# Kernel tuning notes

Measured on AMD Instinct MI355X. Metric: run time of the kernel, lower is better.

## Reference

```python
import jax, jax.numpy as jnp
import numpy as np

B, S, D, H = 64, 65536, 512, 256
H2 = H // 2
CAP_LIMIT = 0.85
ACT_THR = 0.5


def _normalize(x):
    return x / jnp.maximum(jnp.linalg.norm(x, axis=-1, keepdims=True), 1e-12)


def _layernorm(x, g, b):
    m = x.mean(-1, keepdims=True)
    v = ((x - m) ** 2).mean(-1, keepdims=True)
    return (x - m) / jnp.sqrt(v + 1e-5) * g + b


def setup_inputs() -> dict:
    key = jax.random.key(0)
    ks = jax.random.split(key, 20)

    def lin(k, i, o):
        s = 1.0 / np.sqrt(i)
        kw, kb = jax.random.split(k)
        return (jax.random.uniform(kw, (i, o), minval=-s, maxval=s),
                jax.random.uniform(kb, (o,), minval=-s, maxval=s))

    inp = {}
    inp["new_content"] = jax.random.normal(ks[0], (B, D), dtype=jnp.float32)
    inp["query"] = jax.random.normal(ks[1], (B, D), dtype=jnp.float32)
    inp["memory_bank"] = jax.random.normal(ks[2], (S, D), dtype=jnp.float32)
    inp["access_times"] = jax.random.uniform(ks[3], (S,), minval=0.0, maxval=900.0)
    inp["current_step"] = 1000
    inp["sr_w1"], inp["sr_b1"] = lin(ks[4], 2 * D, H)
    inp["sr_g"] = jnp.ones((H,), jnp.float32)
    inp["sr_beta"] = jnp.zeros((H,), jnp.float32)
    inp["sr_w2"], inp["sr_b2"] = lin(ks[5], H, H2)
    inp["sn_w"], inp["sn_b"] = lin(ks[6], D, H2)
    inp["sg_w"], inp["sg_b"] = lin(ks[7], H2, 1)
    inp["el_w"], inp["el_b"] = lin(ks[8], 1, 32)
    inp["ec_w"], inp["ec_b"] = lin(ks[9], D, 32)
    inp["eg_w"], inp["eg_b"] = lin(ks[10], 64, 1)
    inp["dd_w1"], inp["dd_b1"] = lin(ks[11], 2 * D, H)
    inp["dd_w2"], inp["dd_b2"] = lin(ks[12], H, 1)
    inp["ds_w1"], inp["ds_b1"] = lin(ks[13], 2 * D, H)
    inp["ds_w2"], inp["ds_b2"] = lin(ks[14], H, 1)
    return inp


def _forward(new_content, query, memory_bank, access_times,
             sr_w1, sr_b1, sr_g, sr_beta, sr_w2, sr_b2,
             sn_w, sn_b, sg_w, sg_b,
             el_w, el_b, ec_w, ec_b, eg_w, eg_b,
             dd_w1, dd_b1, dd_w2, dd_b2,
             ds_w1, ds_b1, ds_w2, ds_b2,
             step):
    mem = memory_bank
    at = access_times
    norms = jnp.linalg.norm(mem, axis=-1)               # [S]
    capacity = jnp.mean((norms > ACT_THR).astype(jnp.float32))
    dyn_thr = jnp.clip(
        jnp.where(capacity < 0.3, 0.08,
                  jnp.where(capacity < 0.6, 0.08 + (capacity - 0.3) * 0.733,
                            0.3 + (capacity - 0.6))), 0.0, 0.7)
    topk_thr = jnp.where(capacity < 0.3, 0.1, jnp.where(capacity < 0.6, 0.2, 0.4))
    raw_thr = jnp.where(capacity < 0.3, 0.3, 0.5)

    # store relevance / novelty / gate
    combined = jnp.concatenate([new_content, query], -1)          # [B,2D]
    h = _layernorm(combined @ sr_w1 + sr_b1, sr_g, sr_beta)
    rel = jax.nn.relu(jax.nn.relu(h) @ sr_w2 + sr_b2)             # [B,H2]
    nn_ = _normalize(new_content)
    sims = nn_ @ _normalize(mem).T                                # [B,S]
    max_sim = sims.max(-1, keepdims=True)
    novelty = (1.0 - max_sim) / 2.0                               # [B,1]
    nf = jax.nn.sigmoid(new_content @ sn_w + sn_b)
    store_score = jax.nn.sigmoid((rel + nf) @ sg_w + sg_b)        # [B,1]

    # novelty percentile over active slots (no boolean-shape gather)
    active = norms > ACT_THR
    n_active = active.sum()
    nov_mean = novelty.mean()
    cond = (nov_mean > (1.0 - sims)) & active[None, :]
    denom = (new_content.shape[0] * jnp.maximum(n_active, 1)).astype(jnp.float32)
    perc = jnp.where(n_active > 0, cond.sum().astype(jnp.float32) / denom, 1.0)

    base_store = store_score.mean() > raw_thr
    novelty_ok = nov_mean > dyn_thr
    topk_ok = perc > topk_thr
    should_store = base_store & novelty_ok & topk_ok

    # emergency erase (capacity over limit)
    do_erase = capacity > CAP_LIMIT
    age = jnp.maximum(step - at, 0.0)
    es_em = age / (age.max() + 1e-6) + (1.0 - jax.nn.sigmoid(norms))
    victim = jnp.argmax(es_em)
    mem = jnp.where(do_erase, mem.at[victim].set(0.0), mem)
    at = jnp.where(do_erase, at.at[victim].set(-99999.0), at)
    should_store = should_store & jnp.logical_not(do_erase & jnp.logical_not(novelty_ok))

    # per-slot erase scores
    lru = jax.nn.relu(((step - at) / 1000.0)[:, None] @ el_w + el_b)   # [S,32]
    conf = jax.nn.sigmoid(mem @ ec_w + ec_b)                            # [S,32]
    erase_scores = jax.nn.sigmoid(jnp.concatenate([lru, conf], -1) @ eg_w + eg_b)[:, 0]

    # conflict detection: top-3 similar slots, gather-MLP-scatter drift
    sims2 = _normalize(new_content) @ _normalize(mem).T                # [B,S]
    tv, ti = jax.lax.top_k(sims2, 3)                                   # [B,3]
    cmask = (tv > 0.7) & (tv < 0.99)
    gathered = mem[ti]                                                 # [B,3,D]
    pair = jnp.concatenate([jnp.broadcast_to(new_content[:, None, :], gathered.shape), gathered], -1)
    prob = jax.nn.sigmoid(jax.nn.relu(pair @ dd_w1 + dd_b1) @ dd_w2 + dd_b2)[..., 0]
    strength = jax.nn.sigmoid(jax.nn.relu(pair @ ds_w1 + ds_b1) @ ds_w2 + ds_b2)[..., 0]
    apply_m = cmask & (prob > 0.5)                                     # [B,3]
    avg = (new_content[:, None, :] + gathered) / 2.0
    s = strength[..., None]
    dn_cand = (1.0 - s) * new_content[:, None, :] + s * avg
    do_cand = (1.0 - s) * gathered + s * avg
    drifted_new = new_content
    for k in range(3):  # fixed k=3, later k overwrites (matches torch inner loop)
        drifted_new = jnp.where(apply_m[:, k:k + 1], dn_cand[:, k], drifted_new)
    for k in range(3):
        idx = ti[:, k]
        cur = mem[idx]
        mem = mem.at[idx].set(jnp.where(apply_m[:, k, None], do_cand[:, k], cur))

    # conditional write
    slot_age = step - at
    recent = (at >= 0.0) & (slot_age < 3.0)
    masked = erase_scores * (~recent).astype(erase_scores.dtype)
    masked = jnp.where(masked.max() <= 0.0, slot_age, masked)
    write_idx = jnp.where(do_erase, victim, jnp.argmax(masked))
    erase_out = jnp.where(should_store & jnp.logical_not(do_erase), masked, erase_scores)
    mem = jnp.where(should_store, mem.at[write_idx].set(drifted_new[0]), mem)
    at = jnp.where(should_store, at.at[write_idx].set(step), at)

    recent_changes = jnp.abs(mem - memory_bank).mean()
    return (mem, at, erase_out, store_score[:, 0], novelty[:, 0], recent_changes)


def reference(new_content, query, memory_bank, access_times,
              sr_w1, sr_b1, sr_g, sr_beta, sr_w2, sr_b2,
              sn_w, sn_b, sg_w, sg_b,
              el_w, el_b, ec_w, ec_b, eg_w, eg_b,
              dd_w1, dd_b1, dd_w2, dd_b2,
              ds_w1, ds_b1, ds_w2, ds_b2,
              current_step):
    step = jnp.float32(current_step)
    return _forward(new_content, query, memory_bank, access_times,
                    sr_w1, sr_b1, sr_g, sr_beta, sr_w2, sr_b2,
                    sn_w, sn_b, sg_w, sg_b,
                    el_w, el_b, ec_w, ec_b, eg_w, eg_b,
                    dd_w1, dd_b1, dd_w2, dd_b2,
                    ds_w1, ds_b1, ds_w2, ds_b2, step)
```

## Files before the change

### kernel.cpp

```cpp
#include <hip/hip_runtime.h>
#include <math.h>
#include <limits.h>

#define S_N 65536
#define D_N 512
#define B_N 64

typedef __attribute__((ext_vector_type(8))) short short8;
typedef __attribute__((ext_vector_type(4))) float f32x4;

#define SIMS_F      (B_N*S_N/2)
#define OFF_SIMS    0
#define OFF_AEXT    (OFF_SIMS + SIMS_F)
#define AEXT_F      (96*512/2)
#define OFF_NORMS   (OFF_AEXT + AEXT_F)
#define OFF_CONF    (OFF_NORMS + S_N)
#define OFF_FLAGS   (OFF_CONF + S_N)
#define OFF_LIST    (OFF_FLAGS + S_N)
#define OFF_MASKED  (OFF_LIST + 256)
#define OFF_ERSC    (OFF_MASKED + S_N)
#define OFF_SLOTAGE (OFF_ERSC + S_N)
#define OFF_STORES  (OFF_SLOTAGE + S_N)
#define OFF_MAXSIM  (OFF_STORES + 64)
#define OFF_TI      (OFF_MAXSIM + 64)
// ... 55 lines not shown
__device__ __forceinline__ void touch_row(int row, float* ws){
  int* flags = (int*)(ws + OFF_FLAGS);
  if (atomicExch(&flags[row], 1) == 0){
    Scal* sc = (Scal*)(ws + OFF_SCAL);
    int i = atomicAdd(&sc->list_cnt, 1);
    ((int*)(ws + OFF_LIST))[i] = row;
  }
}

__device__ __forceinline__ void gld16(const float* g, void* l){
  __builtin_amdgcn_global_load_lds((const __attribute__((address_space(1))) void*)g,
                                   (__attribute__((address_space(3))) void*)l, 16, 0, 0);
}
#define WAITV(N) asm volatile("s_waitcnt vmcnt(" #N ")" ::: "memory")

__global__ __launch_bounds__(256) void k_init(const float* __restrict__ nc,
                                              const float* __restrict__ at_in,
                                              const float* __restrict__ ec_w,
                                              const int* __restrict__ step_p,
                                              float* __restrict__ ws, float* __restrict__ out){
  int blk = blockIdx.x, t = threadIdx.x;
  Scal* sc = (Scal*)(ws + OFF_SCAL);
  unsigned short* aB = (unsigned short*)(ws + OFF_AEXT);
  if (blk == 0){
    if (t == 0){
      sc->victim_pack = 0ULL; sc->masked_pack = 0ULL; sc->slotage_pack = 0ULL;
      sc->cnt_active = 0; sc->cond_cnt = 0; sc->age_max_t = 0u;
      sc->nov_mean = 0.0f; sc->changed_sum = 0.0f;
      sc->do_erase = 0; sc->should_store = 0; sc->write_idx = 0; sc->victim_idx = 0;
      sc->list_cnt = 0;
    }
    if (t < 64) ((unsigned*)(ws + OFF_MAXSIM))[t] = 0u;
  } else if (blk <= 64){
    int b = blk - 1;
    __shared__ float red[256];
    float x0 = nc[b*512 + t], x1 = nc[b*512 + 256 + t];
    red[t] = x0*x0 + x1*x1;
    __syncthreads();
    for (int o=128;o>0;o>>=1){ if (t<o) red[t]+=red[t+o]; __syncthreads(); }
    float inv = 1.0f / fmaxf(sqrtf(red[0]), 1e-12f);
    aB[b*512 + t]       = bf16r(x0*inv);
    aB[b*512 + 256 + t] = bf16r(x1*inv);
  } else if (blk <= 96){
    int j = blk - 65;
    for (int d=t; d<512; d+=256) aB[(64+j)*512 + d] = bf16r(ec_w[d*32 + j]);
  } else if (blk <= 160){
    int part = blk - 97;
    float stepf = (float)step_p[0];
    float lmax = -1e30f;
    for (int s = part*1024 + t; s < (part+1)*1024; s += 256)
      lmax = fmaxf(lmax, fmaxf(stepf - at_in[s], 0.0f));
    __shared__ float red[256];
    red[t]=lmax; __syncthreads();
    for (int o=128;o>0;o>>=1){ if (t<o) red[t]=fmaxf(red[t],red[t+o]); __syncthreads(); }
    if (t==0) atomicMax(&sc->age_max_t, f2mono(red[0]));
  } else if (blk <= 224){
    int part = blk - 161;
    for (int s = part*1024 + t; s < (part+1)*1024; s += 256)
      out[OUT_AT + s] = at_in[s];
  } else {
    int part = blk - 225;
    int* flags = (int*)(ws + OFF_FLAGS);
    for (int s = part*1024 + t; s < (part+1)*1024; s += 256) flags[s] = 0;
  }
}

__global__ __launch_bounds__(256) void k_phase1(const float* __restrict__ mem,
                                                const float* __restrict__ ec_b,
                                                const float* __restrict__ eg_w,
                                                float* __restrict__ ws, float* __restrict__ out){
  __shared__ __align__(16) unsigned short aT[96*520];
  __shared__ __align__(16) char chunks[4*4*2048];
  __shared__ unsigned lmax[64];
  int t = threadIdx.x;
  int s0 = blockIdx.x * 64;
  Scal* sc = (Scal*)(ws + OFF_SCAL);
  int lane = t & 63, wv = t >> 6;
  int quad = lane >> 4, l15 = lane & 15;
  int row = wv*16 + l15;

  {
    const uint4* src = (const uint4*)(ws + OFF_AEXT);
    #pragma unroll
    for (int i=0;i<24;i++){
      int idx = i*256 + t;
      int arow = idx >> 6, c16 = idx & 63;
      uint4 v = src[idx];
      *(uint4*)((char*)aT + arow*1040 + c16*16) = v;
    }
    if (t < 64) lmax[t] = 0u;
  }
  __syncthreads();

  const float* gsrc = mem + ((size_t)(s0 + row))*512 + quad*8;
  float* od = out + OUT_MEM + ((size_t)(s0 + row))*512 + quad*8;
  char* mybuf = chunks + wv*8192;
  #define STAGE(c) do{ \
    gld16(gsrc + (c)*32,     mybuf + ((c)&3)*2048); \
    gld16(gsrc + (c)*32 + 4, mybuf + ((c)&3)*2048 + 1024); \
  }while(0)

  STAGE(0); asm volatile("" ::: "memory");
  STAGE(1); asm volatile("" ::: "memory");
  STAGE(2); asm volatile("" ::: "memory");

  f32x4 acc[6];
  #pragma unroll
  for (int r=0;r<6;r++) acc[r] = (f32x4){0.f,0.f,0.f,0.f};
  float ssq = 0.f;

  #pragma unroll
  for (int c=0;c<16;c++){
    if (c < 13) STAGE(c+3);
    if      (c == 0)  WAITV(6);
    else if (c == 1)  WAITV(8);
    else if (c == 2)  WAITV(10);
    else if (c <= 12) WAITV(12);
    else if (c == 13) WAITV(10);
    else if (c == 14) WAITV(8);
    else              WAITV(6);
    __builtin_amdgcn_sched_barrier(0);
    const char* bp = mybuf + (c&3)*2048;
    float4 v0 = *(const float4*)(bp + lane*16);
    float4 v1 = *(const float4*)(bp + 1024 + lane*16);
    *(float4*)(od + c*32)     = v0;
    *(float4*)(od + c*32 + 4) = v1;
    ssq = fmaf(v0.x,v0.x,ssq); ssq = fmaf(v0.y,v0.y,ssq);
    ssq = fmaf(v0.z,v0.z,ssq); ssq = fmaf(v0.w,v0.w,ssq);
    ssq = fmaf(v1.x,v1.x,ssq); ssq = fmaf(v1.y,v1.y,ssq);
    ssq = fmaf(v1.z,v1.z,ssq); ssq = fmaf(v1.w,v1.w,ssq);
    short8 bfrag;
    bfrag[0]=(short)bf16r(v0.x); bfrag[1]=(short)bf16r(v0.y);
    bfrag[2]=(short)bf16r(v0.z); bfrag[3]=(short)bf16r(v0.w);
    bfrag[4]=(short)bf16r(v1.x); bfrag[5]=(short)bf16r(v1.y);
    bfrag[6]=(short)bf16r(v1.z); bfrag[7]=(short)bf16r(v1.w);
    #pragma unroll
    for (int rt=0;rt<6;rt++){
      short8 afrag = *(const short8*)&aT[(rt*16 + l15)*520 + c*32 + quad*8];
      acc[rt] = __builtin_amdgcn_mfma_f32_16x16x32_bf16(afrag, bfrag, acc[rt], 0,0,0);
    }
  }
  #undef STAGE

  ssq += __shfl_xor(ssq, 16);
  ssq += __shfl_xor(ssq, 32);
  float nrm = sqrtf(ssq);
  float lv = 1.0f / fmaxf(nrm, 1e-12f);
  if (quad == 0) ws[OFF_NORMS + s0 + row] = nrm;
  unsigned long long m = __ballot(quad==0 && nrm > 0.5f);
  if (lane == 0) atomicAdd(&sc->cnt_active, (int)__popcll(m));

  unsigned short* simsb = (unsigned short*)(ws + OFF_SIMS);
  #pragma unroll
  for (int rt=0;rt<4;rt++){
    #pragma unroll
    for (int r=0;r<4;r++){
      int a = rt*16 + quad*4 + r;
      float sim = acc[rt][r] * lv;
      simsb[(size_t)a*S_N + s0 + row] = bf16r(sim);
      atomicMax(&lmax[a], f2mono(sim));
    }
  }
  float cpart = 0.f;
  #pragma unroll
  for (int rt=4;rt<6;rt++){
    #pragma unroll
    for (int r=0;r<4;r++){
      int j = (rt-4)*16 + quad*4 + r;
      cpart += sigmoidf_(acc[rt][r] + ec_b[j]) * eg_w[32+j];
    }
  }
  cpart += __shfl_down(cpart, 32);
  cpart += __shfl_down(cpart, 16);
  if (lane < 16) ws[OFF_CONF + s0 + row] = cpart;
  __syncthreads();
  if (t < 64) atomicMax(((unsigned*)(ws + OFF_MAXSIM)) + t, lmax[t]);
}

__global__ __launch_bounds__(256) void k_mlp1a(const float* __restrict__ nc, const float* __restrict__ qr,
    const float* __restrict__ sr_w1, float* __restrict__ ws){
  int blk = blockIdx.x, t = threadIdx.x;
  int b = blk >> 1, half = blk & 1;
  __shared__ float ch[512];
  const float* src = half ? qr : nc;
  ch[t] = src[b*512 + t]; ch[256+t] = src[b*512 + 256 + t];
  __syncthreads();
  float h = 0.f;
  const float* w = sr_w1 + (half*512)*256 + t;
  for (int i=0;i<512;i++) h = fmaf(ch[i], w[i*256], h);
  ws[OFF_HM + (half*64 + b)*256 + t] = h;
}

__global__ __launch_bounds__(256) void k_mlp1b(const float* __restrict__ nc, const float* __restrict__ qr,
    const float* __restrict__ sr_b1, const float* __restrict__ sr_g, const float* __restrict__ sr_beta,
    const float* __restrict__ sr_w2, const float* __restrict__ sr_b2,
    const float* __restrict__ sn_w,  const float* __restrict__ sn_b,
    const float* __restrict__ sg_w,  const float* __restrict__ sg_b,
    float* __restrict__ ws, float* __restrict__ out){
  int b = blockIdx.x, t = threadIdx.x;
  Scal* sc = (Scal*)(ws + OFF_SCAL);
  __shared__ float red[256];
  if (b == 64){
    const unsigned* gms = (const unsigned*)(ws + OFF_MAXSIM);
    float nv = 0.0f;
    if (t < 64){
      float msim = mono2f(gms[t]);
      nv = (1.0f - msim) * 0.5f;
      out[OUT_NOV + t] = nv;
    }
    red[t] = (t < 64) ? nv : 0.0f;
    __syncthreads();
    for (int o=128;o>0;o>>=1){ if (t<o) red[t]+=red[t+o]; __syncthreads(); }
    if (t == 0) sc->nov_mean = red[0] / 64.0f;
    return;
  }
  __shared__ float comb[1024];
  __shared__ float hbuf[256];
  comb[t]       = nc[b*512 + t];
  comb[256 + t] = nc[b*512 + 256 + t];
  comb[512 + t] = qr[b*512 + t];
  comb[768 + t] = qr[b*512 + 256 + t];
  float h = ws[OFF_HM + b*256 + t] + ws[OFF_HM + (64 + b)*256 + t] + sr_b1[t];
  red[t] = h; __syncthreads();
  for (int o=128;o>0;o>>=1){ if (t<o) red[t]+=red[t+o]; __syncthreads(); }
  float mean = red[0] / 256.0f;
  __syncthreads();
  float dx = h - mean;
  red[t] = dx*dx; __syncthreads();
  for (int o=128;o>0;o>>=1){ if (t<o) red[t]+=red[t+o]; __syncthreads(); }
  float var = red[0] / 256.0f;
  __syncthreads();
  float hn = dx / sqrtf(var + 1e-5f) * sr_g[t] + sr_beta[t];
  hbuf[t] = fmaxf(hn, 0.0f);
  __syncthreads();
  float val = 0.0f;
  if (t < 128){
    float r = sr_b2[t];
    for (int j=0;j<256;j++) r = fmaf(hbuf[j], sr_w2[j*128 + t], r);
    r = fmaxf(r, 0.0f);
    float nf = sn_b[t];
    for (int d=0; d<512; d++) nf = fmaf(comb[d], sn_w[d*128 + t], nf);
    nf = sigmoidf_(nf);
    val = (r + nf) * sg_w[t];
  }
  red[t] = val; __syncthreads();
  for (int o=128;o>0;o>>=1){ if (t<o) red[t]+=red[t+o]; __syncthreads(); }
  if (t == 0){
    float ssc = sigmoidf_(red[0] + sg_b[0]);
    out[OUT_SS + b] = ssc;
    ws[OFF_STORES + b] = ssc;
  }
}

__global__ __launch_bounds__(256) void k_scan(const float* __restrict__ at_in,
                                              const int* __restrict__ step_p,
                                              float* __restrict__ ws){
  int t = threadIdx.x;
  Scal* sc = (Scal*)(ws + OFF_SCAL);
  float thr = 1.0f - sc->nov_mean;
  float stepf = (float)step_p[0];
  float agemax = mono2f(sc->age_max_t);
  const unsigned* simsu = (const unsigned*)(ws + OFF_SIMS);
  const float* norms = ws + OFF_NORMS;
  int gid = blockIdx.x*256 + t;
  int gstride = gridDim.x*256;
  int cnt = 0;
  for (int idx = gid; idx < B_N*S_N/2; idx += gstride){
    unsigned u = simsu[idx];
    int s = (idx*2) & (S_N-1);
    float v0 = __uint_as_float(u<<16);
    float v1 = __uint_as_float(u & 0xffff0000u);
    if (v0 > thr && norms[s]   > 0.5f) cnt++;
    if (v1 > thr && norms[s+1] > 0.5f) cnt++;
  }
  unsigned long long best = 0ULL;
  for (int s = gid; s < S_N; s += gstride){
    float age = fmaxf(stepf - at_in[s], 0.0f);
    float es = age/(agemax + 1e-6f) + (1.0f - sigmoidf_(norms[s]));
    unsigned long long pk = packvi(es, s);
    if (pk > best) best = pk;
  }
  __shared__ int redc[256];
  __shared__ unsigned long long redp[256];
  redc[t] = cnt; redp[t] = best;
  __syncthreads();
  for (int o=128;o>0;o>>=1){
    if (t<o){ redc[t]+=redc[t+o]; if (redp[t+o] > redp[t]) redp[t]=redp[t+o]; }
    __syncthreads();
  }
  if (t == 0){
    atomicAdd(&sc->cond_cnt, redc[0]);
    atomicMax(&sc->victim_pack, redp[0]);
  }
}

__global__ __launch_bounds__(256) void k_victimfix(const float* __restrict__ ec_b,
                                                   const float* __restrict__ eg_w,
                                                   float* __restrict__ ws, float* __restrict__ out){
  int t = threadIdx.x;
  Scal* sc = (Scal*)(ws + OFF_SCAL);
  float capacity = (float)sc->cnt_active / 65536.0f;
  int de = (capacity > 0.85f) ? 1 : 0;
  int victim = (int)(0xFFFFFFFFu - (unsigned)(sc->victim_pack & 0xFFFFFFFFULL));
  if (t == 0){ sc->do_erase = de; sc->victim_idx = victim; }
  if (de){
    for (int d=t; d<512; d+=256) out[OUT_MEM + victim*512 + d] = 0.0f;
    if (t == 0){
      out[OUT_AT + victim] = -99999.0f;
      touch_row(victim, ws);
      float sum = 0.0f;
      for (int j=0;j<32;j++) sum += sigmoidf_(ec_b[j]) * eg_w[32 + j];
      ws[OFF_CONF + victim] = sum;
    }
  }
}

__global__ __launch_bounds__(256) void k_top3(float* __restrict__ ws){
  int b = blockIdx.x, t = threadIdx.x;
  Scal* sc = (Scal*)(ws + OFF_SCAL);
  int de = sc->do_erase;
  int victim = sc->victim_idx;
  const unsigned short* simrow = (const unsigned short*)(ws + OFF_SIMS) + (size_t)b*S_N;
  float v[3] = {-1e30f,-1e30f,-1e30f};
  int ix[3] = {INT_MAX, INT_MAX, INT_MAX};
  for (int s = t; s < S_N; s += 256){
    float val = bf2f(simrow[s]);
    if (de && s == victim) val = 0.0f;
    if (betterVI(val, s, v[2], ix[2])){
      if (betterVI(val, s, v[1], ix[1])){
        if (betterVI(val, s, v[0], ix[0])){
          v[2]=v[1]; ix[2]=ix[1]; v[1]=v[0]; ix[1]=ix[0]; v[0]=val; ix[0]=s;
        } else { v[2]=v[1]; ix[2]=ix[1]; v[1]=val; ix[1]=s; }
      } else { v[2]=val; ix[2]=s; }
    }
  }
  __shared__ float sv[256*3];
  __shared__ int   si[256*3];
  for (int r=0;r<3;r++){ sv[t*3+r]=v[r]; si[t*3+r]=ix[r]; }
  for (int off=128; off>0; off>>=1){
    __syncthreads();
    if (t < off){
      float av[3], bv[3], ov[3]; int ai[3], bi[3], oi[3];
      for (int r=0;r<3;r++){ av[r]=sv[t*3+r]; ai[r]=si[t*3+r]; bv[r]=sv[(t+off)*3+r]; bi[r]=si[(t+off)*3+r]; }
      int ap=0, bp=0;
      for (int r=0;r<3;r++){
        bool takeA = (bp>=3) || (ap<3 && betterVI(av[ap],ai[ap],bv[bp],bi[bp]));
        if (takeA){ ov[r]=av[ap]; oi[r]=ai[ap]; ap++; }
        else      { ov[r]=bv[bp]; oi[r]=bi[bp]; bp++; }
      }
      for (int r=0;r<3;r++){ sv[t*3+r]=ov[r]; si[t*3+r]=oi[r]; }
    }
  }
  __syncthreads();
  if (t == 0){
    for (int k=0;k<3;k++){
      ws[OFF_TV + b*3 + k] = sv[k];
      ((int*)(ws + OFF_TI))[b*3 + k] = si[k];
    }
  }
}

__global__ __launch_bounds__(256) void k_mlp2(const float* __restrict__ nc,
    const float* __restrict__ dd_w1, const float* __restrict__ ds_w1,
    float* __restrict__ ws, float* __restrict__ out){
  int blk = blockIdx.x, t = threadIdx.x;
  int b = blk >> 2, ks = blk & 3;
  __shared__ float ch[3*256];
  if (ks < 2){
    ch[t] = nc[b*512 + ks*256 + t];
    __syncthreads();
    float hd = 0.f, hs = 0.f;
    const float* wd = dd_w1 + (ks*256)*256 + t;
// ... 62 lines not shown
  float tvv = ws[OFF_TV + p];
  int ap = (tvv > 0.7f && tvv < 0.99f && prob > 0.5f) ? 1 : 0;
  if (t == 0){
    ((int*)(ws + OFF_APPLY))[p] = ap;
    touch_row(row, ws);
  }
  for (int d=t; d<512; d+=256){
    float n = nc[b*512 + d];
    float g = out[OUT_MEM + (size_t)row*512 + d];
    float avg = 0.5f*(n + g);
    ws[OFF_DOCAND + p*512 + d] = (1.0f - stren)*g + stren*avg;
    if (b == 0) ws[OFF_DNC0 + k*512 + d] = (1.0f - stren)*n + stren*avg;
  }
}

__global__ __launch_bounds__(64) void k_scatter(float* __restrict__ ws, float* __restrict__ out){
  int d = blockIdx.x*64 + threadIdx.x;
  const int* tip = (const int*)(ws + OFF_TI);
  const int* ap  = (const int*)(ws + OFF_APPLY);
  for (int k=0;k<3;k++){
    float cur[64];
    #pragma unroll
    for (int b=0;b<64;b++) cur[b] = out[OUT_MEM + (size_t)tip[b*3 + k]*512 + d];
    #pragma unroll
    for (int b=0;b<64;b++){
      int p = b*3 + k;
      float v = ap[p] ? ws[OFF_DOCAND + p*512 + d] : cur[b];
      out[OUT_MEM + (size_t)tip[p]*512 + d] = v;
    }
  }
}

__global__ __launch_bounds__(256) void k_erase(const int* __restrict__ step_p,
    const float* __restrict__ el_w, const float* __restrict__ el_b,
    const float* __restrict__ eg_w, const float* __restrict__ eg_b,
    float* __restrict__ ws, float* __restrict__ out){
  int t = threadIdx.x;
  Scal* sc = (Scal*)(ws + OFF_SCAL);
  float stepf = (float)step_p[0];
  float egb = eg_b[0];
  int gid = blockIdx.x*256 + t;
  int gstride = gridDim.x*256;
  unsigned long long bm = 0ULL, bs = 0ULL;
  for (int s = gid; s < S_N; s += gstride){
    float a = out[OUT_AT + s];
    float x = (stepf - a) / 1000.0f;
    float lp = 0.0f;
    #pragma unroll
    for (int j=0;j<32;j++) lp += fmaxf(x*el_w[j] + el_b[j], 0.0f) * eg_w[j];
    float er = sigmoidf_(lp + ws[OFF_CONF + s] + egb);
    float sa = stepf - a;
    bool recent = (a >= 0.0f) && (sa < 3.0f);
    float msk = recent ? 0.0f : er;
    ws[OFF_ERSC + s] = er;
    ws[OFF_MASKED + s] = msk;
    ws[OFF_SLOTAGE + s] = sa;
    unsigned long long pm = packvi(msk, s); if (pm > bm) bm = pm;
    unsigned long long ps = packvi(sa,  s); if (ps > bs) bs = ps;
  }
  __shared__ unsigned long long rm[256], rs[256];
  rm[t]=bm; rs[t]=bs; __syncthreads();
  for (int o=128;o>0;o>>=1){
    if (t<o){ if (rm[t+o]>rm[t]) rm[t]=rm[t+o]; if (rs[t+o]>rs[t]) rs[t]=rs[t+o]; }
    __syncthreads();
  }
  if (t == 0){
    atomicMax(&sc->masked_pack, rm[0]);
    atomicMax(&sc->slotage_pack, rs[0]);
  }
}

__global__ __launch_bounds__(64) void k_decide(const float* __restrict__ nc, float* __restrict__ ws){
  int t = threadIdx.x;
  Scal* sc = (Scal*)(ws + OFF_SCAL);
  __shared__ float red[64];
  red[t] = ws[OFF_STORES + t];
  __syncthreads();
  for (int o=32;o>0;o>>=1){ if (t<o) red[t]+=red[t+o]; __syncthreads(); }
  if (t == 0){
    float store_mean = red[0] / 64.0f;
    int cnt = sc->cnt_active;
    float capacity = (float)cnt / 65536.0f;
    float dyn_thr;
    if (capacity < 0.3f) dyn_thr = 0.08f;
    else if (capacity < 0.6f) dyn_thr = 0.08f + (capacity - 0.3f)*0.733f;
    else dyn_thr = 0.3f + (capacity - 0.6f);
    dyn_thr = fminf(fmaxf(dyn_thr, 0.0f), 0.7f);
    float topk_thr = (capacity < 0.3f) ? 0.1f : ((capacity < 0.6f) ? 0.2f : 0.4f);
    float raw_thr  = (capacity < 0.3f) ? 0.3f : 0.5f;
    int base_store = store_mean > raw_thr;
    int novelty_ok = sc->nov_mean > dyn_thr;
    int cmax = cnt > 1 ? cnt : 1;
    float denom = (float)(64 * cmax);
    float perc = (cnt > 0) ? ((float)sc->cond_cnt) / denom : 1.0f;
    int topk_ok = perc > topk_thr;
    int de = sc->do_erase;
    int ss = base_store && novelty_ok && topk_ok;
    if (de && !novelty_ok) ss = 0;
    float mmax = mono2f((unsigned)(sc->masked_pack >> 32));
    int marg = (int)(0xFFFFFFFFu - (unsigned)(sc->masked_pack  & 0xFFFFFFFFULL));
    int sarg = (int)(0xFFFFFFFFu - (unsigned)(sc->slotage_pack & 0xFFFFFFFFULL));
    sc->should_store = ss;
    sc->write_idx = de ? sc->victim_idx : ((mmax > 0.0f) ? marg : sarg);
  }
  __syncthreads();
  const int* ap = (const int*)(ws + OFF_APPLY);
  for (int d=t; d<512; d+=64){
    float v = nc[d];
    if (ap[0]) v = ws[OFF_DNC0 + 0*512 + d];
    if (ap[1]) v = ws[OFF_DNC0 + 1*512 + d];
    if (ap[2]) v = ws[OFF_DNC0 + 2*512 + d];
    ws[OFF_DRIFT0 + d] = v;
  }
}

__global__ __launch_bounds__(256) void k_finalout(const int* __restrict__ step_p,
                                                  float* __restrict__ ws, float* __restrict__ out){
  int blk = blockIdx.x, t = threadIdx.x;
  Scal* sc = (Scal*)(ws + OFF_SCAL);
  int ss = sc->should_store, de = sc->do_erase;
  if (blk == 64){
    if (ss){
      int wi = sc->write_idx;
      for (int d=t; d<512; d+=256) out[OUT_MEM + (size_t)wi*512 + d] = ws[OFF_DRIFT0 + d];
      if (t == 0){
        out[OUT_AT + wi] = (float)step_p[0];
        touch_row(wi, ws);
      }
    }
    return;
  }
  float mmax = mono2f((unsigned)(sc->masked_pack >> 32));
  bool usemask = ss && !de;
  for (int s = blk*256 + t; s < S_N; s += 64*256){
    float v;
    if (usemask) v = (mmax <= 0.0f) ? ws[OFF_SLOTAGE + s] : ws[OFF_MASKED + s];
    else v = ws[OFF_ERSC + s];
    out[OUT_ER + s] = v;
  }
// ... 4 lines not shown
  int t = threadIdx.x;
  Scal* sc = (Scal*)(ws + OFF_SCAL);
  int cnt = sc->list_cnt;
  const int* list = (const int*)(ws + OFF_LIST);
  float lsum = 0.0f;
  for (int i = blockIdx.x; i < cnt; i += gridDim.x){
    int row = list[i];
    float part = 0.0f;
    for (int d=t; d<512; d+=256)
      part += fabsf(out[OUT_MEM + (size_t)row*512 + d] - mem[(size_t)row*512 + d]);
    lsum += part;
  }
  __shared__ float red[256];
  red[t] = lsum; __syncthreads();
  for (int o=128;o>0;o>>=1){ if (t<o) red[t]+=red[t+o]; __syncthreads(); }
  if (t == 0 && red[0] != 0.0f) atomicAdd(&sc->changed_sum, red[0]);
}

__global__ void k_rc(float* __restrict__ ws, float* __restrict__ out){
  if (threadIdx.x == 0 && blockIdx.x == 0){
    Scal* sc = (Scal*)(ws + OFF_SCAL);
    out[OUT_RC] = sc->changed_sum / 33554432.0f;
  }
}

extern "C" void kernel_launch(void* const* d_in, const int* in_sizes, int n_in,
                              void* d_out, int out_size, void* d_ws, size_t ws_size,
                              hipStream_t stream) {
  const float* nc    = (const float*)d_in[0];
  const float* qr    = (const float*)d_in[1];
  const float* mem   = (const float*)d_in[2];
  const float* at    = (const float*)d_in[3];
  const int*   step  = (const int*)  d_in[4];
  const float* sr_w1 = (const float*)d_in[5];
  const float* sr_b1 = (const float*)d_in[6];
  const float* sr_g  = (const float*)d_in[7];
  const float* sr_be = (const float*)d_in[8];
  const float* sr_w2 = (const float*)d_in[9];
// ... 7 lines not shown
  const float* ec_w  = (const float*)d_in[17];
  const float* ec_b  = (const float*)d_in[18];
  const float* eg_w  = (const float*)d_in[19];
  const float* eg_b  = (const float*)d_in[20];
  const float* dd_w1 = (const float*)d_in[21];
  const float* dd_b1 = (const float*)d_in[22];
  const float* dd_w2 = (const float*)d_in[23];
  const float* dd_b2 = (const float*)d_in[24];
  const float* ds_w1 = (const float*)d_in[25];
  const float* ds_b1 = (const float*)d_in[26];
  const float* ds_w2 = (const float*)d_in[27];
  const float* ds_b2 = (const float*)d_in[28];
  float* out = (float*)d_out;
  float* ws  = (float*)d_ws;

  k_init     <<<dim3(289), dim3(256), 0, stream>>>(nc, at, ec_w, step, ws, out);
  k_mlp1a    <<<dim3(128), dim3(256), 0, stream>>>(nc, qr, sr_w1, ws);
  k_phase1   <<<dim3(1024), dim3(256), 0, stream>>>(mem, ec_b, eg_w, ws, out);
  k_mlp1b    <<<dim3(65), dim3(256), 0, stream>>>(nc, qr, sr_b1, sr_g, sr_be,
                                                  sr_w2, sr_b2, sn_w, sn_b, sg_w, sg_b, ws, out);
  k_scan     <<<dim3(512), dim3(256), 0, stream>>>(at, step, ws);
  k_victimfix<<<dim3(1), dim3(256), 0, stream>>>(ec_b, eg_w, ws, out);
  k_top3     <<<dim3(64), dim3(256), 0, stream>>>(ws);
  k_mlp2     <<<dim3(256), dim3(256), 0, stream>>>(nc, dd_w1, ds_w1, ws, out);
  k_pairfin  <<<dim3(192), dim3(256), 0, stream>>>(nc, dd_b1, dd_w2, dd_b2,
                                                   ds_b1, ds_w2, ds_b2, ws, out);
  k_scatter  <<<dim3(8), dim3(64), 0, stream>>>(ws, out);
  k_erase    <<<dim3(64), dim3(256), 0, stream>>>(step, el_w, el_b, eg_w, eg_b, ws, out);
  k_decide   <<<dim3(1), dim3(64), 0, stream>>>(nc, ws);
  k_finalout <<<dim3(65), dim3(256), 0, stream>>>(step, ws, out);
  k_diff     <<<dim3(64), dim3(256), 0, stream>>>(mem, ws, out);
  k_rc       <<<dim3(1), dim3(64), 0, stream>>>(ws, out);
}
```

Baseline: 557.0 us.

## Merge small kernels and move victim scoring into the phase-1 GEMM

Cuts the launch count from fifteen to eight by fusing several independent small kernels into multi-role launches: mlp1a into init; mlp1b, victimfix, scan and top3 into one mid kernel; scatter with erase; decide with finalout; rc folded into diff via an atomic add on the output. The victim erase-score argmax now runs inside phase1, removing a pass over norms and access times. Phase1 moves to 512-thread blocks covering 128 rows each, with a three-deep staging ring instead of four. Fusing roles whose results depend on each other into one launch risks ordering hazards, for example the victim fix reading counters that other blocks of the same launch are still producing.

```diff
diff --git a/kernel.cpp b/kernel.cpp
--- a/kernel.cpp
+++ b/kernel.cpp
@@ -93,14 +93,18 @@
 }
 #define WAITV(N) asm volatile("s_waitcnt vmcnt(" #N ")" ::: "memory")
 
-__global__ __launch_bounds__(256) void k_init(const float* __restrict__ nc,
-                                              const float* __restrict__ at_in,
-                                              const float* __restrict__ ec_w,
-                                              const int* __restrict__ step_p,
-                                              float* __restrict__ ws, float* __restrict__ out){
+__global__ __launch_bounds__(256) void k_initm(const float* __restrict__ nc,
+                                               const float* __restrict__ qr,
+                                               const float* __restrict__ at_in,
+                                               const float* __restrict__ ec_w,
+                                               const int* __restrict__ step_p,
+                                               const float* __restrict__ sr_w1,
+                                               float* __restrict__ ws, float* __restrict__ out){
   int blk = blockIdx.x, t = threadIdx.x;
   Scal* sc = (Scal*)(ws + OFF_SCAL);
   unsigned short* aB = (unsigned short*)(ws + OFF_AEXT);
+  __shared__ float red[256];
+  __shared__ float ch[512];
   if (blk == 0){
     if (t == 0){
       sc->victim_pack = 0ULL; sc->masked_pack = 0ULL; sc->slotage_pack = 0ULL;
@@ -108,11 +112,11 @@
       sc->nov_mean = 0.0f; sc->changed_sum = 0.0f;
       sc->do_erase = 0; sc->should_store = 0; sc->write_idx = 0; sc->victim_idx = 0;
       sc->list_cnt = 0;
+      out[OUT_RC] = 0.0f;
     }
     if (t < 64) ((unsigned*)(ws + OFF_MAXSIM))[t] = 0u;
   } else if (blk <= 64){
     int b = blk - 1;
-    __shared__ float red[256];
     float x0 = nc[b*512 + t], x1 = nc[b*512 + 256 + t];
     red[t] = x0*x0 + x1*x1;
     __syncthreads();
@@ -126,33 +130,44 @@
   } else if (blk <= 160){
     int part = blk - 97;
     float stepf = (float)step_p[0];
-    float lmax = -1e30f;
+    float lmaxv = -1e30f;
     for (int s = part*1024 + t; s < (part+1)*1024; s += 256)
-      lmax = fmaxf(lmax, fmaxf(stepf - at_in[s], 0.0f));
-    __shared__ float red[256];
-    red[t]=lmax; __syncthreads();
+      lmaxv = fmaxf(lmaxv, fmaxf(stepf - at_in[s], 0.0f));
+    red[t]=lmaxv; __syncthreads();
     for (int o=128;o>0;o>>=1){ if (t<o) red[t]=fmaxf(red[t],red[t+o]); __syncthreads(); }
     if (t==0) atomicMax(&sc->age_max_t, f2mono(red[0]));
   } else if (blk <= 224){
     int part = blk - 161;
     for (int s = part*1024 + t; s < (part+1)*1024; s += 256)
       out[OUT_AT + s] = at_in[s];
-  } else {
+  } else if (blk <= 288){
     int part = blk - 225;
     int* flags = (int*)(ws + OFF_FLAGS);
     for (int s = part*1024 + t; s < (part+1)*1024; s += 256) flags[s] = 0;
-  }
-}
-
-__global__ __launch_bounds__(256) void k_phase1(const float* __restrict__ mem,
+  } else {
+    int blk2 = blk - 289;
+    int b = blk2 >> 1, half = blk2 & 1;
+    const float* src = half ? qr : nc;
+    ch[t] = src[b*512 + t]; ch[256+t] = src[b*512 + 256 + t];
+    __syncthreads();
+    float h = 0.f;
+    const float* w = sr_w1 + (half*512)*256 + t;
+    for (int i=0;i<512;i++) h = fmaf(ch[i], w[i*256], h);
+    ws[OFF_HM + (half*64 + b)*256 + t] = h;
+  }
+}
+
+__global__ __launch_bounds__(512) void k_phase1(const float* __restrict__ mem,
+                                                const float* __restrict__ at_in,
+                                                const int* __restrict__ step_p,
                                                 const float* __restrict__ ec_b,
                                                 const float* __restrict__ eg_w,
                                                 float* __restrict__ ws, float* __restrict__ out){
   __shared__ __align__(16) unsigned short aT[96*520];
-  __shared__ __align__(16) char chunks[4*4*2048];
+  __shared__ __align__(16) char chunks[8*3*2048];
   __shared__ unsigned lmax[64];
   int t = threadIdx.x;
-  int s0 = blockIdx.x * 64;
+  int s0 = blockIdx.x * 128;
   Scal* sc = (Scal*)(ws + OFF_SCAL);
   int lane = t & 63, wv = t >> 6;
   int quad = lane >> 4, l15 = lane & 15;
@@ -161,8 +176,8 @@
   {
     const uint4* src = (const uint4*)(ws + OFF_AEXT);
     #pragma unroll
-    for (int i=0;i<24;i++){
-      int idx = i*256 + t;
+    for (int i=0;i<12;i++){
+      int idx = i*512 + t;
       int arow = idx >> 6, c16 = idx & 63;
       uint4 v = src[idx];
       *(uint4*)((char*)aT + arow*1040 + c16*16) = v;
@@ -173,15 +188,14 @@
 
   const float* gsrc = mem + ((size_t)(s0 + row))*512 + quad*8;
   float* od = out + OUT_MEM + ((size_t)(s0 + row))*512 + quad*8;
-  char* mybuf = chunks + wv*8192;
+  char* mybuf = chunks + wv*6144;
   #define STAGE(c) do{ \
-    gld16(gsrc + (c)*32,     mybuf + ((c)&3)*2048); \
-    gld16(gsrc + (c)*32 + 4, mybuf + ((c)&3)*2048 + 1024); \
+    gld16(gsrc + (c)*32,     mybuf + ((c)%3)*2048); \
+    gld16(gsrc + (c)*32 + 4, mybuf + ((c)%3)*2048 + 1024); \
   }while(0)
 
   STAGE(0); asm volatile("" ::: "memory");
   STAGE(1); asm volatile("" ::: "memory");
-  STAGE(2); asm volatile("" ::: "memory");
 
   f32x4 acc[6];
   #pragma unroll
@@ -190,16 +204,14 @@
 
   #pragma unroll
   for (int c=0;c<16;c++){
-    if (c < 13) STAGE(c+3);
-    if      (c == 0)  WAITV(6);
-    else if (c == 1)  WAITV(8);
-    else if (c == 2)  WAITV(10);
-    else if (c <= 12) WAITV(12);
-    else if (c == 13) WAITV(10);
-    else if (c == 14) WAITV(8);
-    else              WAITV(6);
+    if (c < 14) STAGE(c+2);
+    if      (c == 0)  WAITV(4);
+    else if (c == 1)  WAITV(6);
+    else if (c <= 13) WAITV(8);
+    else if (c == 14) WAITV(6);
+    else              WAITV(4);
     __builtin_amdgcn_sched_barrier(0);
-    const char* bp = mybuf + (c&3)*2048;
+    const char* bp = mybuf + (c%3)*2048;
     float4 v0 = *(const float4*)(bp + lane*16);
     float4 v1 = *(const float4*)(bp + 1024 + lane*16);
     *(float4*)(od + c*32)     = v0;
@@ -215,7 +227,7 @@
     bfrag[6]=(short)bf16r(v1.z); bfrag[7]=(short)bf16r(v1.w);
     #pragma unroll
     for (int rt=0;rt<6;rt++){
-      short8 afrag = *(const short8*)&aT[(rt*16 + l15)*520 + c*32 + quad*8];
+      short8 afrag = *(const short8*)((const char*)aT + (rt*16 + l15)*1040 + c*64 + quad*16);
       acc[rt] = __builtin_amdgcn_mfma_f32_16x16x32_bf16(afrag, bfrag, acc[rt], 0,0,0);
     }
   }
@@ -228,6 +240,23 @@
   if (quad == 0) ws[OFF_NORMS + s0 + row] = nrm;
   unsigned long long m = __ballot(quad==0 && nrm > 0.5f);
   if (lane == 0) atomicAdd(&sc->cnt_active, (int)__popcll(m));
+
+  {
+    float agemax = mono2f(sc->age_max_t);
+    float stepf = (float)step_p[0];
+    unsigned long long pk = 0ULL;
+    if (quad == 0){
+      float age = fmaxf(stepf - at_in[s0 + row], 0.0f);
+      float es = age/(agemax + 1e-6f) + (1.0f - sigmoidf_(nrm));
+      pk = packvi(es, s0 + row);
+    }
+    #pragma unroll
+    for (int o=32;o>0;o>>=1){
+      unsigned long long other = __shfl_xor(pk, o);
+      if (other > pk) pk = other;
+    }
+    if (lane == 0) atomicMax(&sc->victim_pack, pk);
+  }
 
   unsigned short* simsb = (unsigned short*)(ws + OFF_SIMS);
   #pragma unroll
@@ -256,30 +285,22 @@
   if (t < 64) atomicMax(((unsigned*)(ws + OFF_MAXSIM)) + t, lmax[t]);
 }
 
-__global__ __launch_bounds__(256) void k_mlp1a(const float* __restrict__ nc, const float* __restrict__ qr,
-    const float* __restrict__ sr_w1, float* __restrict__ ws){
-  int blk = blockIdx.x, t = threadIdx.x;
-  int b = blk >> 1, half = blk & 1;
-  __shared__ float ch[512];
-  const float* src = half ? qr : nc;
-  ch[t] = src[b*512 + t]; ch[256+t] = src[b*512 + 256 + t];
-  __syncthreads();
-  float h = 0.f;
-  const float* w = sr_w1 + (half*512)*256 + t;
-  for (int i=0;i<512;i++) h = fmaf(ch[i], w[i*256], h);
-  ws[OFF_HM + (half*64 + b)*256 + t] = h;
-}
-
-__global__ __launch_bounds__(256) void k_mlp1b(const float* __restrict__ nc, const float* __restrict__ qr,
+__global__ __launch_bounds__(256) void k_mid(const float* __restrict__ nc, const float* __restrict__ qr,
     const float* __restrict__ sr_b1, const float* __restrict__ sr_g, const float* __restrict__ sr_beta,
     const float* __restrict__ sr_w2, const float* __restrict__ sr_b2,
     const float* __restrict__ sn_w,  const float* __restrict__ sn_b,
     const float* __restrict__ sg_w,  const float* __restrict__ sg_b,
+    const float* __restrict__ ec_b,  const float* __restrict__ eg_w,
     float* __restrict__ ws, float* __restrict__ out){
-  int b = blockIdx.x, t = threadIdx.x;
+  int blk = blockIdx.x, t = threadIdx.x;
   Scal* sc = (Scal*)(ws + OFF_SCAL);
   __shared__ float red[256];
-  if (b == 64){
+  __shared__ float comb[1024];
+  __shared__ float hbuf[256];
+  __shared__ float sv[256*3];
+  __shared__ int   si[256*3];
+
+  if (blk == 64){
     const unsigned* gms = (const unsigned*)(ws + OFF_MAXSIM);
     float nv = 0.0f;
     if (t < 64){
@@ -293,148 +314,127 @@
     if (t == 0) sc->nov_mean = red[0] / 64.0f;
     return;
   }
-  __shared__ float comb[1024];
-  __shared__ float hbuf[256];
-  comb[t]       = nc[b*512 + t];
-  comb[256 + t] = nc[b*512 + 256 + t];
-  comb[512 + t] = qr[b*512 + t];
-  comb[768 + t] = qr[b*512 + 256 + t];
-  float h = ws[OFF_HM + b*256 + t] + ws[OFF_HM + (64 + b)*256 + t] + sr_b1[t];
-  red[t] = h; __syncthreads();
-  for (int o=128;o>0;o>>=1){ if (t<o) red[t]+=red[t+o]; __syncthreads(); }
-  float mean = red[0] / 256.0f;
-  __syncthreads();
-  float dx = h - mean;
-  red[t] = dx*dx; __syncthreads();
-  for (int o=128;o>0;o>>=1){ if (t<o) red[t]+=red[t+o]; __syncthreads(); }
-  float var = red[0] / 256.0f;
-  __syncthreads();
-  float hn = dx / sqrtf(var + 1e-5f) * sr_g[t] + sr_beta[t];
-  hbuf[t] = fmaxf(hn, 0.0f);
-  __syncthreads();
-  float val = 0.0f;
-  if (t < 128){
-    float r = sr_b2[t];
-    for (int j=0;j<256;j++) r = fmaf(hbuf[j], sr_w2[j*128 + t], r);
-    r = fmaxf(r, 0.0f);
-    float nf = sn_b[t];
-    for (int d=0; d<512; d++) nf = fmaf(comb[d], sn_w[d*128 + t], nf);
-    nf = sigmoidf_(nf);
-    val = (r + nf) * sg_w[t];
-  }
-  red[t] = val; __syncthreads();
-  for (int o=128;o>0;o>>=1){ if (t<o) red[t]+=red[t+o]; __syncthreads(); }
-  if (t == 0){
-    float ssc = sigmoidf_(red[0] + sg_b[0]);
-    out[OUT_SS + b] = ssc;
-    ws[OFF_STORES + b] = ssc;
-  }
-}
-
-__global__ __launch_bounds__(256) void k_scan(const float* __restrict__ at_in,
-                                              const int* __restrict__ step_p,
-                                              float* __restrict__ ws){
-  int t = threadIdx.x;
-  Scal* sc = (Scal*)(ws + OFF_SCAL);
-  float thr = 1.0f - sc->nov_mean;
-  float stepf = (float)step_p[0];
-  float agemax = mono2f(sc->age_max_t);
-  const unsigned* simsu = (const unsigned*)(ws + OFF_SIMS);
-  const float* norms = ws + OFF_NORMS;
-  int gid = blockIdx.x*256 + t;
-  int gstride = gridDim.x*256;
-  int cnt = 0;
-  for (int idx = gid; idx < B_N*S_N/2; idx += gstride){
-    unsigned u = simsu[idx];
-    int s = (idx*2) & (S_N-1);
-    float v0 = __uint_as_float(u<<16);
-    float v1 = __uint_as_float(u & 0xffff0000u);
-    if (v0 > thr && norms[s]   > 0.5f) cnt++;
-    if (v1 > thr && norms[s+1] > 0.5f) cnt++;
-  }
-  unsigned long long best = 0ULL;
-  for (int s = gid; s < S_N; s += gstride){
-    float age = fmaxf(stepf - at_in[s], 0.0f);
-    float es = age/(agemax + 1e-6f) + (1.0f - sigmoidf_(norms[s]));
-    unsigned long long pk = packvi(es, s);
-    if (pk > best) best = pk;
-  }
-  __shared__ int redc[256];
-  __shared__ unsigned long long redp[256];
-  redc[t] = cnt; redp[t] = best;
-  __syncthreads();
-  for (int o=128;o>0;o>>=1){
-    if (t<o){ redc[t]+=redc[t+o]; if (redp[t+o] > redp[t]) redp[t]=redp[t+o]; }
-    __syncthreads();
-  }
-  if (t == 0){
-    atomicAdd(&sc->cond_cnt, redc[0]);
-    atomicMax(&sc->victim_pack, redp[0]);
-  }
-}
-
-__global__ __launch_bounds__(256) void k_victimfix(const float* __restrict__ ec_b,
-                                                   const float* __restrict__ eg_w,
-                                                   float* __restrict__ ws, float* __restrict__ out){
-  int t = threadIdx.x;
-  Scal* sc = (Scal*)(ws + OFF_SCAL);
-  float capacity = (float)sc->cnt_active / 65536.0f;
-  int de = (capacity > 0.85f) ? 1 : 0;
-  int victim = (int)(0xFFFFFFFFu - (unsigned)(sc->victim_pack & 0xFFFFFFFFULL));
-  if (t == 0){ sc->do_erase = de; sc->victim_idx = victim; }
-  if (de){
-    for (int d=t; d<512; d+=256) out[OUT_MEM + victim*512 + d] = 0.0f;
+  if (blk < 64){
+    int b = blk;
+    comb[t]       = nc[b*512 + t];
+    comb[256 + t] = nc[b*512 + 256 + t];
+    comb[512 + t] = qr[b*512 + t];
+    comb[768 + t] = qr[b*512 + 256 + t];
+    float h = ws[OFF_HM + b*256 + t] + ws[OFF_HM + (64 + b)*256 + t] + sr_b1[t];
+    red[t] = h; __syncthreads();
+    for (int o=128;o>0;o>>=1){ if (t<o) red[t]+=red[t+o]; __syncthreads(); }
+    float mean = red[0] / 256.0f;
+    __syncthreads();
+    float dx = h - mean;
+    red[t] = dx*dx; __syncthreads();
+    for (int o=128;o>0;o>>=1){ if (t<o) red[t]+=red[t+o]; __syncthreads(); }
+    float var = red[0] / 256.0f;
+    __syncthreads();
+    float hn = dx / sqrtf(var + 1e-5f) * sr_g[t] + sr_beta[t];
+    hbuf[t] = fmaxf(hn, 0.0f);
+    __syncthreads();
+    float val = 0.0f;
+    if (t < 128){
+      float r = sr_b2[t];
+      for (int j=0;j<256;j++) r = fmaf(hbuf[j], sr_w2[j*128 + t], r);
+      r = fmaxf(r, 0.0f);
+      float nf = sn_b[t];
+      for (int d=0; d<512; d++) nf = fmaf(comb[d], sn_w[d*128 + t], nf);
+      nf = sigmoidf_(nf);
+      val = (r + nf) * sg_w[t];
+    }
+    red[t] = val; __syncthreads();
+    for (int o=128;o>0;o>>=1){ if (t<o) red[t]+=red[t+o]; __syncthreads(); }
     if (t == 0){
-      out[OUT_AT + victim] = -99999.0f;
-      touch_row(victim, ws);
-      float sum = 0.0f;
-      for (int j=0;j<32;j++) sum += sigmoidf_(ec_b[j]) * eg_w[32 + j];
-      ws[OFF_CONF + victim] = sum;
-    }
-  }
-}
-
-__global__ __launch_bounds__(256) void k_top3(float* __restrict__ ws){
-  int b = blockIdx.x, t = threadIdx.x;
-  Scal* sc = (Scal*)(ws + OFF_SCAL);
-  int de = sc->do_erase;
-  int victim = sc->victim_idx;
-  const unsigned short* simrow = (const unsigned short*)(ws + OFF_SIMS) + (size_t)b*S_N;
-  float v[3] = {-1e30f,-1e30f,-1e30f};
-  int ix[3] = {INT_MAX, INT_MAX, INT_MAX};
-  for (int s = t; s < S_N; s += 256){
-    float val = bf2f(simrow[s]);
-    if (de && s == victim) val = 0.0f;
-    if (betterVI(val, s, v[2], ix[2])){
-      if (betterVI(val, s, v[1], ix[1])){
-        if (betterVI(val, s, v[0], ix[0])){
-          v[2]=v[1]; ix[2]=ix[1]; v[1]=v[0]; ix[1]=ix[0]; v[0]=val; ix[0]=s;
-        } else { v[2]=v[1]; ix[2]=ix[1]; v[1]=val; ix[1]=s; }
-      } else { v[2]=val; ix[2]=s; }
-    }
-  }
-  __shared__ float sv[256*3];
-  __shared__ int   si[256*3];
-  for (int r=0;r<3;r++){ sv[t*3+r]=v[r]; si[t*3+r]=ix[r]; }
-  for (int off=128; off>0; off>>=1){
-    __syncthreads();
-    if (t < off){
-      float av[3], bv[3], ov[3]; int ai[3], bi[3], oi[3];
-      for (int r=0;r<3;r++){ av[r]=sv[t*3+r]; ai[r]=si[t*3+r]; bv[r]=sv[(t+off)*3+r]; bi[r]=si[(t+off)*3+r]; }
-      int ap=0, bp=0;
-      for (int r=0;r<3;r++){
-        bool takeA = (bp>=3) || (ap<3 && betterVI(av[ap],ai[ap],bv[bp],bi[bp]));
-        if (takeA){ ov[r]=av[ap]; oi[r]=ai[ap]; ap++; }
-        else      { ov[r]=bv[bp]; oi[r]=bi[bp]; bp++; }
+      float ssc = sigmoidf_(red[0] + sg_b[0]);
+      out[OUT_SS + b] = ssc;
+      ws[OFF_STORES + b] = ssc;
+    }
+    return;
+  }
+  if (blk == 65){
+    float capacity = (float)sc->cnt_active / 65536.0f;
+    int de = (capacity > 0.85f) ? 1 : 0;
+    int victim = (int)(0xFFFFFFFFu - (unsigned)(sc->victim_pack & 0xFFFFFFFFULL));
+    if (t == 0){ sc->do_erase = de; sc->victim_idx = victim; }
+    if (de){
+      for (int d=t; d<512; d+=256) out[OUT_MEM + victim*512 + d] = 0.0f;
+      if (t == 0){
+        out[OUT_AT + victim] = -99999.0f;
+        touch_row(victim, ws);
+        float sum = 0.0f;
+        for (int j=0;j<32;j++) sum += sigmoidf_(ec_b[j]) * eg_w[32 + j];
+        ws[OFF_CONF + victim] = sum;
       }
-      for (int r=0;r<3;r++){ sv[t*3+r]=ov[r]; si[t*3+r]=oi[r]; }
-    }
-  }
-  __syncthreads();
-  if (t == 0){
-    for (int k=0;k<3;k++){
-      ws[OFF_TV + b*3 + k] = sv[k];
-      ((int*)(ws + OFF_TI))[b*3 + k] = si[k];
+    }
+    return;
+  }
+  if (blk < 578){
+    const unsigned* gms = (const unsigned*)(ws + OFF_MAXSIM);
+    red[t] = (t < 64) ? (1.0f - mono2f(gms[t])) * 0.5f : 0.0f;
+    __syncthreads();
+    for (int o=128;o>0;o>>=1){ if (t<o) red[t]+=red[t+o]; __syncthreads(); }
+    float thr = 1.0f - red[0] / 64.0f;
+    const unsigned* simsu = (const unsigned*)(ws + OFF_SIMS);
+    const float* norms = ws + OFF_NORMS;
+    int gid = (blk - 66)*256 + t;
+    int gstride = 512*256;
+    int cnt = 0;
+    for (int idx = gid; idx < B_N*S_N/2; idx += gstride){
+      unsigned u = simsu[idx];
+      int s = (idx*2) & (S_N-1);
+      float v0 = __uint_as_float(u<<16);
+      float v1 = __uint_as_float(u & 0xffff0000u);
+      if (v0 > thr && norms[s]   > 0.5f) cnt++;
+      if (v1 > thr && norms[s+1] > 0.5f) cnt++;
+    }
+    __syncthreads();
+    int* redc = (int*)red;
+    redc[t] = cnt;
+    __syncthreads();
+    for (int o=128;o>0;o>>=1){ if (t<o) redc[t]+=redc[t+o]; __syncthreads(); }
+    if (t == 0) atomicAdd(&sc->cond_cnt, redc[0]);
+    return;
+  }
+  {
+    int b = blk - 578;
+    int victim = (int)(0xFFFFFFFFu - (unsigned)(sc->victim_pack & 0xFFFFFFFFULL));
+    int de = (((float)sc->cnt_active / 65536.0f) > 0.85f) ? 1 : 0;
+    const unsigned short* simrow = (const unsigned short*)(ws + OFF_SIMS) + (size_t)b*S_N;
+    float v[3] = {-1e30f,-1e30f,-1e30f};
+    int ix[3] = {INT_MAX, INT_MAX, INT_MAX};
+    for (int s = t; s < S_N; s += 256){
+      float val = bf2f(simrow[s]);
+      if (de && s == victim) val = 0.0f;
+      if (betterVI(val, s, v[2], ix[2])){
+        if (betterVI(val, s, v[1], ix[1])){
+          if (betterVI(val, s, v[0], ix[0])){
+            v[2]=v[1]; ix[2]=ix[1]; v[1]=v[0]; ix[1]=ix[0]; v[0]=val; ix[0]=s;
+          } else { v[2]=v[1]; ix[2]=ix[1]; v[1]=val; ix[1]=s; }
+        } else { v[2]=val; ix[2]=s; }
+      }
+    }
+    for (int r=0;r<3;r++){ sv[t*3+r]=v[r]; si[t*3+r]=ix[r]; }
+    for (int off=128; off>0; off>>=1){
+      __syncthreads();
+      if (t < off){
+        float av[3], bv[3], ov[3]; int ai[3], bi[3], oi[3];
+        for (int r=0;r<3;r++){ av[r]=sv[t*3+r]; ai[r]=si[t*3+r]; bv[r]=sv[(t+off)*3+r]; bi[r]=si[(t+off)*3+r]; }
+        int ap=0, bp=0;
+        for (int r=0;r<3;r++){
+          bool takeA = (bp>=3) || (ap<3 && betterVI(av[ap],ai[ap],bv[bp],bi[bp]));
+          if (takeA){ ov[r]=av[ap]; oi[r]=ai[ap]; ap++; }
+          else      { ov[r]=bv[bp]; oi[r]=bi[bp]; bp++; }
+        }
+        for (int r=0;r<3;r++){ sv[t*3+r]=ov[r]; si[t*3+r]=oi[r]; }
+      }
+    }
+    __syncthreads();
+    if (t == 0){
+      for (int k=0;k<3;k++){
+        ws[OFF_TV + b*3 + k] = sv[k];
+        ((int*)(ws + OFF_TI))[b*3 + k] = si[k];
+      }
     }
   }
 }
@@ -527,33 +527,34 @@
   }
 }
 
-__global__ __launch_bounds__(64) void k_scatter(float* __restrict__ ws, float* __restrict__ out){
-  int d = blockIdx.x*64 + threadIdx.x;
-  const int* tip = (const int*)(ws + OFF_TI);
-  const int* ap  = (const int*)(ws + OFF_APPLY);
-  for (int k=0;k<3;k++){
-    float cur[64];
-    #pragma unroll
-    for (int b=0;b<64;b++) cur[b] = out[OUT_MEM + (size_t)tip[b*3 + k]*512 + d];
-    #pragma unroll
-    for (int b=0;b<64;b++){
-      int p = b*3 + k;
-      float v = ap[p] ? ws[OFF_DOCAND + p*512 + d] : cur[b];
-      out[OUT_MEM + (size_t)tip[p]*512 + d] = v;
-    }
-  }
-}
-
-__global__ __launch_bounds__(256) void k_erase(const int* __restrict__ step_p,
+__global__ __launch_bounds__(256) void k_scer(const int* __restrict__ step_p,
     const float* __restrict__ el_w, const float* __restrict__ el_b,
     const float* __restrict__ eg_w, const float* __restrict__ eg_b,
     float* __restrict__ ws, float* __restrict__ out){
-  int t = threadIdx.x;
+  int blk = blockIdx.x, t = threadIdx.x;
   Scal* sc = (Scal*)(ws + OFF_SCAL);
+  __shared__ unsigned long long rm[256], rs[256];
+  if (blk < 2){
+    int d = blk*256 + t;
+    const int* tip = (const int*)(ws + OFF_TI);
+    const int* ap  = (const int*)(ws + OFF_APPLY);
+    for (int k=0;k<3;k++){
+      float cur[64];
+      #pragma unroll
+      for (int b=0;b<64;b++) cur[b] = out[OUT_MEM + (size_t)tip[b*3 + k]*512 + d];
+      #pragma unroll
+      for (int b=0;b<64;b++){
+        int p = b*3 + k;
+        float v = ap[p] ? ws[OFF_DOCAND + p*512 + d] : cur[b];
+        out[OUT_MEM + (size_t)tip[p]*512 + d] = v;
+      }
+    }
+    return;
+  }
   float stepf = (float)step_p[0];
   float egb = eg_b[0];
-  int gid = blockIdx.x*256 + t;
-  int gstride = gridDim.x*256;
+  int gid = (blk-2)*256 + t;
+  int gstride = 64*256;
   unsigned long long bm = 0ULL, bs = 0ULL;
   for (int s = gid; s < S_N; s += gstride){
     float a = out[OUT_AT + s];
@@ -571,7 +572,6 @@
     unsigned long long pm = packvi(msk, s); if (pm > bm) bm = pm;
     unsigned long long ps = packvi(sa,  s); if (ps > bs) bs = ps;
   }
-  __shared__ unsigned long long rm[256], rs[256];
   rm[t]=bm; rs[t]=bs; __syncthreads();
   for (int o=128;o>0;o>>=1){
     if (t<o){ if (rm[t+o]>rm[t]) rm[t]=rm[t+o]; if (rs[t+o]>rs[t]) rs[t]=rs[t+o]; }
@@ -583,11 +583,14 @@
   }
 }
 
-__global__ __launch_bounds__(64) void k_decide(const float* __restrict__ nc, float* __restrict__ ws){
-  int t = threadIdx.x;
+__global__ __launch_bounds__(256) void k_finalout(const float* __restrict__ nc,
+                                                  const int* __restrict__ step_p,
+                                                  float* __restrict__ ws, float* __restrict__ out){
+  int blk = blockIdx.x, t = threadIdx.x;
   Scal* sc = (Scal*)(ws + OFF_SCAL);
   __shared__ float red[64];
-  red[t] = ws[OFF_STORES + t];
+  __shared__ int sh_ss, sh_wi;
+  if (t < 64) red[t] = ws[OFF_STORES + t];
   __syncthreads();
   for (int o=32;o>0;o>>=1){ if (t<o) red[t]+=red[t+o]; __syncthreads(); }
   if (t == 0){
@@ -613,29 +616,22 @@
     float mmax = mono2f((unsigned)(sc->masked_pack >> 32));
     int marg = (int)(0xFFFFFFFFu - (unsigned)(sc->masked_pack  & 0xFFFFFFFFULL));
     int sarg = (int)(0xFFFFFFFFu - (unsigned)(sc->slotage_pack & 0xFFFFFFFFULL));
-    sc->should_store = ss;
-    sc->write_idx = de ? sc->victim_idx : ((mmax > 0.0f) ? marg : sarg);
+    sh_ss = ss;
+    sh_wi = de ? sc->victim_idx : ((mmax > 0.0f) ? marg : sarg);
   }
   __syncthreads();
-  const int* ap = (const int*)(ws + OFF_APPLY);
-  for (int d=t; d<512; d+=64){
-    float v = nc[d];
-    if (ap[0]) v = ws[OFF_DNC0 + 0*512 + d];
-    if (ap[1]) v = ws[OFF_DNC0 + 1*512 + d];
-    if (ap[2]) v = ws[OFF_DNC0 + 2*512 + d];
-    ws[OFF_DRIFT0 + d] = v;
-  }
-}
-
-__global__ __launch_bounds__(256) void k_finalout(const int* __restrict__ step_p,
-                                                  float* __restrict__ ws, float* __restrict__ out){
-  int blk = blockIdx.x, t = threadIdx.x;
-  Scal* sc = (Scal*)(ws + OFF_SCAL);
-  int ss = sc->should_store, de = sc->do_erase;
+  int ss = sh_ss, de = sc->do_erase;
   if (blk == 64){
     if (ss){
-      int wi = sc->write_idx;
-      for (int d=t; d<512; d+=256) out[OUT_MEM + (size_t)wi*512 + d] = ws[OFF_DRIFT0 + d];
+      int wi = sh_wi;
+      const int* ap = (const int*)(ws + OFF_APPLY);
+      for (int d=t; d<512; d+=256){
+        float v = nc[d];
+        if (ap[0]) v = ws[OFF_DNC0 + 0*512 + d];
+        if (ap[1]) v = ws[OFF_DNC0 + 1*512 + d];
+        if (ap[2]) v = ws[OFF_DNC0 + 2*512 + d];
+        out[OUT_MEM + (size_t)wi*512 + d] = v;
+      }
       if (t == 0){
         out[OUT_AT + wi] = (float)step_p[0];
         touch_row(wi, ws);
@@ -670,14 +666,7 @@
   __shared__ float red[256];
   red[t] = lsum; __syncthreads();
   for (int o=128;o>0;o>>=1){ if (t<o) red[t]+=red[t+o]; __syncthreads(); }
-  if (t == 0 && red[0] != 0.0f) atomicAdd(&sc->changed_sum, red[0]);
-}
-
-__global__ void k_rc(float* __restrict__ ws, float* __restrict__ out){
-  if (threadIdx.x == 0 && blockIdx.x == 0){
-    Scal* sc = (Scal*)(ws + OFF_SCAL);
-    out[OUT_RC] = sc->changed_sum / 33554432.0f;
-  }
+  if (t == 0 && red[0] != 0.0f) atomicAdd(out + OUT_RC, red[0] * (1.0f/33554432.0f));
 }
 
 extern "C" void kernel_launch(void* const* d_in, const int* in_sizes, int n_in,
@@ -715,21 +704,15 @@
   float* out = (float*)d_out;
   float* ws  = (float*)d_ws;
 
-  k_init     <<<dim3(289), dim3(256), 0, stream>>>(nc, at, ec_w, step, ws, out);
-  k_mlp1a    <<<dim3(128), dim3(256), 0, stream>>>(nc, qr, sr_w1, ws);
-  k_phase1   <<<dim3(1024), dim3(256), 0, stream>>>(mem, ec_b, eg_w, ws, out);
-  k_mlp1b    <<<dim3(65), dim3(256), 0, stream>>>(nc, qr, sr_b1, sr_g, sr_be,
-                                                  sr_w2, sr_b2, sn_w, sn_b, sg_w, sg_b, ws, out);
-  k_scan     <<<dim3(512), dim3(256), 0, stream>>>(at, step, ws);
-  k_victimfix<<<dim3(1), dim3(256), 0, stream>>>(ec_b, eg_w, ws, out);
-  k_top3     <<<dim3(64), dim3(256), 0, stream>>>(ws);
+  k_initm    <<<dim3(417), dim3(256), 0, stream>>>(nc, qr, at, ec_w, step, sr_w1, ws, out);
+  k_phase1   <<<dim3(512), dim3(512), 0, stream>>>(mem, at, step, ec_b, eg_w, ws, out);
+  k_mid      <<<dim3(642), dim3(256), 0, stream>>>(nc, qr, sr_b1, sr_g, sr_be,
+                                                   sr_w2, sr_b2, sn_w, sn_b, sg_w, sg_b,
+                                                   ec_b, eg_w, ws, out);
   k_mlp2     <<<dim3(256), dim3(256), 0, stream>>>(nc, dd_w1, ds_w1, ws, out);
   k_pairfin  <<<dim3(192), dim3(256), 0, stream>>>(nc, dd_b1, dd_w2, dd_b2,
                                                    ds_b1, ds_w2, ds_b2, ws, out);
-  k_scatter  <<<dim3(8), dim3(64), 0, stream>>>(ws, out);
-  k_erase    <<<dim3(64), dim3(256), 0, stream>>>(step, el_w, el_b, eg_w, eg_b, ws, out);
-  k_decide   <<<dim3(1), dim3(64), 0, stream>>>(nc, ws);
-  k_finalout <<<dim3(65), dim3(256), 0, stream>>>(step, ws, out);
+  k_scer     <<<dim3(66), dim3(256), 0, stream>>>(step, el_w, el_b, eg_w, eg_b, ws, out);
+  k_finalout <<<dim3(65), dim3(256), 0, stream>>>(nc, step, ws, out);
   k_diff     <<<dim3(64), dim3(256), 0, stream>>>(mem, ws, out);
-  k_rc       <<<dim3(1), dim3(64), 0, stream>>>(ws, out);
-}
+}
```

After: 773.7 us. 1.39x slower.
